# Kernel optimization log

Hardware: AMD Instinct MI355X
Metric: run time of the kernel (lower is better)

## Reference

```python
import jax, jax.numpy as jnp
import numpy as np

EMBED = 768
HEADS = 12
B, S = 32, 1024


def setup_inputs() -> dict:
    key = jax.random.key(0)
    k1, k2, k3 = jax.random.split(key, 3)
    scale_in = 1.0 / np.sqrt(EMBED)
    x = jax.random.normal(k1, (B, S, EMBED), dtype=jnp.float32)
    # weights stored [in, out] (transpose of torch Linear layout)
    w_qkv = jax.random.normal(k2, (EMBED, 3 * EMBED), dtype=jnp.float32) * scale_in
    b_qkv = jnp.zeros((3 * EMBED,), dtype=jnp.float32)
    w_o = jax.random.normal(k3, (EMBED, EMBED), dtype=jnp.float32) * scale_in
    b_o = jnp.zeros((EMBED,), dtype=jnp.float32)
    return {"x": x, "w_qkv": w_qkv, "b_qkv": b_qkv, "w_o": w_o, "b_o": b_o}


def reference(x, w_qkv, b_qkv, w_o, b_o):
    Bt, St, E = x.shape
    H = HEADS
    Dh = E // H
    qkv = x @ w_qkv + b_qkv                      # [B, S, 3E]
    qkv = qkv.reshape(Bt, St, H, 3 * Dh)          # [B, S, H, 3Dh]
    q, k, v = jnp.split(qkv, 3, axis=-1)          # each [B, S, H, Dh]
    # NOTE: faithful to source — attention over the HEADS axis per token,
    # scaled by embed_size**-0.5 (not head_dim**-0.5).
    attn = jnp.einsum('bshd,bsgd->bshg', q, k) * (E ** -0.5)  # [B, S, H, H]
    attn = jax.nn.softmax(attn, axis=-1)
    out = jnp.einsum('bshg,bsgd->bshd', attn, v)  # [B, S, H, Dh]
    out = out.reshape(Bt, St, E)
    return out @ w_o + b_o
```

## Files before the change

kernel.cpp:

```cpp
#include <hip/hip_runtime.h>
#include <hip/hip_bf16.h>

#define EMBED 768
#define HEADS 12
#define TOKENS 32768
#define QKVN  (3*EMBED)
#define KDIM  768
#define NKT   (KDIM/64)
#define QK_SCALE 0.03608439182435161f

typedef __attribute__((ext_vector_type(8))) __bf16 bf16x8;
typedef __attribute__((ext_vector_type(4))) __bf16 bf16x4;
typedef __attribute__((ext_vector_type(4))) float  f32x4;

__device__ __forceinline__ void gload_lds16(const void* gptr, void* lptr) {
    __builtin_amdgcn_global_load_lds(
        (const __attribute__((address_space(1))) void*)gptr,
        (__attribute__((address_space(3))) void*)lptr,
        16, 0, 0);
}

__global__ __launch_bounds__(256) void k_cvt_bf16(const float4* __restrict__ src,
                                                  bf16x4* __restrict__ dst, int n4) {
    int i = blockIdx.x * blockDim.x + threadIdx.x;
    int stride = gridDim.x * blockDim.x;
    for (; i < n4; i += stride) {
        float4 f = src[i];
        bf16x4 o;
        o[0] = (__bf16)f.x; o[1] = (__bf16)f.y; o[2] = (__bf16)f.z; o[3] = (__bf16)f.w;
        dst[i] = o;
    }
}

__global__ __launch_bounds__(256) void k_pack_b(const float* __restrict__ w,
                                                __bf16* __restrict__ BF, int N) {
    int tid = blockIdx.x * 256 + threadIdx.x;
    int lane = tid & 63;
    int rest = tid >> 6;
    int N16 = N >> 4;
    int ks = rest & 1;
    int n16 = (rest >> 1) % N16;
    int kt = (rest >> 1) / N16;
    if (kt >= NKT) return;
    int col = n16 * 16 + (lane & 15);
    int k0 = kt * 64 + ks * 32 + (lane >> 4) * 8;
    bf16x8 o;
#pragma unroll
    for (int e = 0; e < 8; ++e) o[e] = (__bf16)w[(size_t)(k0 + e) * N + col];
    *(bf16x8*)(BF + (size_t)tid * 8) = o;
}

template <typename OutT>
__global__ __launch_bounds__(256, 2) void gemm_bl(const __bf16* __restrict__ A,
                                                  const __bf16* __restrict__ BF,
                                                  const float* __restrict__ bias,
                                                  OutT* __restrict__ C, int N) {
    __shared__ __align__(1024) char lds[49152];
    const int tid = threadIdx.x;
    const int w = tid >> 6, lane = tid & 63;
    const int l15 = lane & 15, l16 = lane >> 4;
    const int K = KDIM;
    const int N16 = N >> 4;
    const long ktstride = (long)N16 * 1024;

    const int nbx = N >> 8;
    const int cpx = gridDim.x >> 3;
    const int bid = blockIdx.x;
    const int swz = (bid & 7) * cpx + (bid >> 3);
    const int brow = swz / nbx, bcol = swz % nbx;
    const long arow0 = (long)brow * 128;
    const int  ncol0 = bcol * 256;

    const __bf16* Asrc = A + (arow0 + w * 8 + (lane >> 3)) * K
                           + (((lane & 7) ^ (lane >> 3)) * 8);
    auto stageA = [&](int slot, int kt) {
#pragma unroll
        for (int j = 0; j < 4; ++j)
            gload_lds16(Asrc + (long)(j * 32) * K + (long)kt * 64,
                        lds + slot * 16384 + j * 4096 + w * 1024 + lane * 16);
    };

    const int cA0 = l15 * 128 + (((0 * 4 + l16) ^ (l15 & 7)) * 16);
    const int cA1 = l15 * 128 + (((1 * 4 + l16) ^ (l15 & 7)) * 16);

    const __bf16* bbase = BF + (size_t)lane * 8 + ((long)(ncol0 >> 4) + w * 4) * 1024;

    f32x4 acc[8][4] = {};
    bf16x8 bfv[8];

#define LOADB(KT, HALF) do { \
    _Pragma("unroll") for (int n = 0; n < 4; ++n) \
        bfv[(HALF) * 4 + n] = *(const bf16x8*)(bbase + (long)(KT) * ktstride + n * 1024 + (HALF) * 512); \
} while (0)

#define VMW12 asm volatile("s_waitcnt vmcnt(12)" ::: "memory")
#define VMW8  asm volatile("s_waitcnt vmcnt(8)"  ::: "memory")

#define KSTEP(SLOT, BKT, AKT, VMW, DOBAR) do { \
    bf16x8 af[16]; \
    _Pragma("unroll") for (int mf = 0; mf < 8; ++mf) \
        af[mf] = *(const bf16x8*)(lds + (SLOT) * 16384 + mf * 2048 + cA0); \
    _Pragma("unroll") for (int mf = 0; mf < 8; ++mf) \
        af[8 + mf] = *(const bf16x8*)(lds + (SLOT) * 16384 + mf * 2048 + cA1); \
    __builtin_amdgcn_s_setprio(1); \
    _Pragma("unroll") for (int mf = 0; mf < 8; ++mf) \
        _Pragma("unroll") for (int n = 0; n < 4; ++n) \
            acc[mf][n] = __builtin_amdgcn_mfma_f32_16x16x32_bf16(af[mf], bfv[n], acc[mf][n], 0, 0, 0); \
    __builtin_amdgcn_s_setprio(0); \
    if ((BKT) >= 0) LOADB(BKT, 0); \
    __builtin_amdgcn_s_setprio(1); \
    _Pragma("unroll") for (int mf = 0; mf < 8; ++mf) \
        _Pragma("unroll") for (int n = 0; n < 4; ++n) \
            acc[mf][n] = __builtin_amdgcn_mfma_f32_16x16x32_bf16(af[8 + mf], bfv[4 + n], acc[mf][n], 0, 0, 0); \
    __builtin_amdgcn_s_setprio(0); \
    if ((BKT) >= 0) LOADB(BKT, 1); \
    if ((AKT) >= 0) stageA((AKT) % 3, (AKT)); \
    VMW; \
    if (DOBAR) { __builtin_amdgcn_s_barrier(); __builtin_amdgcn_sched_barrier(0); } \
} while (0)

    stageA(0, 0);
    LOADB(0, 0); LOADB(0, 1);
    asm volatile("s_waitcnt vmcnt(0)" ::: "memory");
    stageA(1, 1);
    __builtin_amdgcn_s_barrier();
    __builtin_amdgcn_sched_barrier(0);

    for (int t = 0; t < 9; t += 3) {
        KSTEP(0, t + 1, t + 2, VMW12, 1);
        KSTEP(1, t + 2, t + 3, VMW12, 1);
        KSTEP(2, t + 3, t + 4, VMW12, 1);
    }
    KSTEP(0, 10, 11, VMW12, 1);
    KSTEP(1, 11, -1, VMW8, 1);
    KSTEP(2, -1, -1, , 0);
#undef KSTEP
#undef LOADB
#undef VMW12
#undef VMW8

#pragma unroll
    for (int mf = 0; mf < 8; ++mf) {
        const int row = (int)arow0 + mf * 16 + l16 * 4;
#pragma unroll
        for (int n = 0; n < 4; ++n) {
            const int col = ncol0 + w * 64 + n * 16 + l15;
            const float bv = bias[col];
#pragma unroll
            for (int j = 0; j < 4; ++j) {
                C[(long)(row + j) * N + col] = (OutT)(acc[mf][n][j] + bv);
            }
        }
    }
}

#define HPITCH 200
__global__ __launch_bounds__(256) void k_attn(const __bf16* __restrict__ qkv,
                                              __bf16* __restrict__ out) {
    __shared__ __bf16 rows[4][12 * HPITCH];
    __shared__ float wts[4][144];
    const int w = threadIdx.x >> 6, lane = threadIdx.x & 63;
    const long token = (long)blockIdx.x * 4 + w;
    const __bf16* rp = qkv + token * QKVN;
    __bf16* row = rows[w];
    float* wt  = wts[w];

#pragma unroll
    for (int i = 0; i < 4; i++) {
        int c = i * 64 + lane;
        int h = c / 24;
        *(bf16x8*)(row + h * HPITCH + (c * 8 - h * 192)) = *(const bf16x8*)(rp + c * 8);
    }
    if (lane < 32) {
        int c = 256 + lane;
        int h = c / 24;
        *(bf16x8*)(row + h * HPITCH + (c * 8 - h * 192)) = *(const bf16x8*)(rp + c * 8);
    }
    __syncthreads();

    for (int p = lane; p < 144; p += 64) {
        int h = p / 12, g = p - h * 12;
        const __bf16* qp = row + h * HPITCH;
        const __bf16* kp = row + g * HPITCH + 64;
        float s = 0.f;
#pragma unroll
        for (int d = 0; d < 64; d += 8) {
            bf16x8 qv = *(const bf16x8*)(qp + d);
            bf16x8 kv = *(const bf16x8*)(kp + d);
#pragma unroll
            for (int j = 0; j < 8; j++) s += (float)qv[j] * (float)kv[j];
        }
        wt[p] = s * QK_SCALE;
    }
    __syncthreads();

    if (lane < 12) {
        float s[12];
#pragma unroll
        for (int g = 0; g < 12; g++) s[g] = wt[lane * 12 + g];
        float m = s[0];
#pragma unroll
        for (int g = 1; g < 12; g++) m = fmaxf(m, s[g]);
        float sum = 0.f;
#pragma unroll
        for (int g = 0; g < 12; g++) { s[g] = __expf(s[g] - m); sum += s[g]; }
        float inv = 1.0f / sum;
#pragma unroll
        for (int g = 0; g < 12; g++) wt[lane * 12 + g] = s[g] * inv;
    }
    __syncthreads();

    float vr[12];
#pragma unroll
    for (int g = 0; g < 12; g++) vr[g] = (float)row[g * HPITCH + 128 + lane];
#pragma unroll
    for (int h = 0; h < 12; h++) {
        float a = 0.f;
#pragma unroll
        for (int g = 0; g < 12; g++) a += wt[h * 12 + g] * vr[g];
        out[token * EMBED + h * 64 + lane] = (__bf16)a;
    }
}

extern "C" void kernel_launch(void* const* d_in, const int* in_sizes, int n_in,
                              void* d_out, int out_size, void* d_ws, size_t ws_size,
                              hipStream_t stream) {
    const float* x     = (const float*)d_in[0];
    const float* w_qkv = (const float*)d_in[1];
    const float* b_qkv = (const float*)d_in[2];
    const float* w_o   = (const float*)d_in[3];
    const float* b_o   = (const float*)d_in[4];
    float* out = (float*)d_out;

    char* ws = (char*)d_ws;
    size_t off = 0;
    auto take = [&](size_t bytes) {
        char* p = ws + off;
        off += (bytes + 255) & ~(size_t)255;
        return p;
    };
    __bf16* wqkvp = (__bf16*)take((size_t)QKVN * KDIM * 2);
    __bf16* wop   = (__bf16*)take((size_t)EMBED * KDIM * 2);
    __bf16* xb    = (__bf16*)take((size_t)TOKENS * EMBED * 2);
    __bf16* qkvb  = (__bf16*)take((size_t)TOKENS * QKVN * 2);
    __bf16* attno = xb;

    int n4 = TOKENS * EMBED / 4;
    k_cvt_bf16<<<2048, 256, 0, stream>>>((const float4*)x, (bf16x4*)xb, n4);

    k_pack_b<<<(NKT * (QKVN / 16) * 2 * 64) / 256, 256, 0, stream>>>(w_qkv, wqkvp, QKVN);
    k_pack_b<<<(NKT * (EMBED / 16) * 2 * 64) / 256, 256, 0, stream>>>(w_o, wop, EMBED);

    gemm_bl<__bf16><<<(TOKENS / 128) * (QKVN / 256), 256, 0, stream>>>(
        xb, wqkvp, b_qkv, qkvb, QKVN);

    k_attn<<<TOKENS / 4, 256, 0, stream>>>(qkvb, attno);

    gemm_bl<float><<<(TOKENS / 128) * (EMBED / 256), 256, 0, stream>>>(
        attno, wop, b_o, out, EMBED);
}
```

Baseline: 237.4 us.

## Fuse fp32-to-bf16 input conversion into the QKV GEMM A-tile staging

Removes the separate conversion kernel for x. The QKV GEMM now reads fp32 activations straight into registers, converts them to bf16 and writes them to LDS, with a software-pipelined three-slot schedule. This saves one full pass over x (read fp32, write bf16) and one kernel launch. In exchange, the GEMM reads twice as many A bytes per tile and each of the 9 column blocks rereads the same rows, adding register pressure and replacing the async global-to-LDS loads with a synchronous register path.

```diff
diff --git a/kernel.cpp b/kernel.cpp
--- a/kernel.cpp
+++ b/kernel.cpp
@@ -18,18 +18,6 @@
         (const __attribute__((address_space(1))) void*)gptr,
         (__attribute__((address_space(3))) void*)lptr,
         16, 0, 0);
-}
-
-__global__ __launch_bounds__(256) void k_cvt_bf16(const float4* __restrict__ src,
-                                                  bf16x4* __restrict__ dst, int n4) {
-    int i = blockIdx.x * blockDim.x + threadIdx.x;
-    int stride = gridDim.x * blockDim.x;
-    for (; i < n4; i += stride) {
-        float4 f = src[i];
-        bf16x4 o;
-        o[0] = (__bf16)f.x; o[1] = (__bf16)f.y; o[2] = (__bf16)f.z; o[3] = (__bf16)f.w;
-        dst[i] = o;
-    }
 }
 
 __global__ __launch_bounds__(256) void k_pack_b(const float* __restrict__ w,
@@ -50,6 +38,129 @@
     *(bf16x8*)(BF + (size_t)tid * 8) = o;
 }
 
+__global__ __launch_bounds__(256, 2) void gemm_cf(const float* __restrict__ A,
+                                                  const __bf16* __restrict__ BF,
+                                                  const float* __restrict__ bias,
+                                                  __bf16* __restrict__ C, int N) {
+    __shared__ __align__(1024) char lds[49152];
+    const int tid = threadIdx.x;
+    const int w = tid >> 6, lane = tid & 63;
+    const int l15 = lane & 15, l16 = lane >> 4;
+    const int K = KDIM;
+    const int N16 = N >> 4;
+    const long ktstride = (long)N16 * 1024;
+
+    const int nbx = N >> 8;
+    const int cpx = gridDim.x >> 3;
+    const int bid = blockIdx.x;
+    const int swz = (bid & 7) * cpx + (bid >> 3);
+    const int brow = swz / nbx, bcol = swz % nbx;
+    const long arow0 = (long)brow * 128;
+    const int  ncol0 = bcol * 256;
+
+    const float* Afsrc = A + (arow0 + w * 8 + (lane >> 3)) * (long)K
+                           + (((lane & 7) ^ (lane >> 3)) * 8);
+    float4 areg[8];
+
+#define ALOAD(KT) do { \
+    _Pragma("unroll") for (int j = 0; j < 4; ++j) { \
+        areg[j * 2]     = *(const float4*)(Afsrc + (long)(j * 32) * K + (long)(KT) * 64); \
+        areg[j * 2 + 1] = *(const float4*)(Afsrc + (long)(j * 32) * K + (long)(KT) * 64 + 4); \
+    } \
+} while (0)
+
+#define AWRITE(SLOT) do { \
+    _Pragma("unroll") for (int j = 0; j < 4; ++j) { \
+        bf16x8 o; \
+        o[0] = (__bf16)areg[j * 2].x;     o[1] = (__bf16)areg[j * 2].y; \
+        o[2] = (__bf16)areg[j * 2].z;     o[3] = (__bf16)areg[j * 2].w; \
+        o[4] = (__bf16)areg[j * 2 + 1].x; o[5] = (__bf16)areg[j * 2 + 1].y; \
+        o[6] = (__bf16)areg[j * 2 + 1].z; o[7] = (__bf16)areg[j * 2 + 1].w; \
+        *(bf16x8*)(lds + (SLOT) * 16384 + j * 4096 + w * 1024 + lane * 16) = o; \
+    } \
+} while (0)
+
+    const int cA0 = l15 * 128 + (((0 * 4 + l16) ^ (l15 & 7)) * 16);
+    const int cA1 = l15 * 128 + (((1 * 4 + l16) ^ (l15 & 7)) * 16);
+    const __bf16* bbase = BF + (size_t)lane * 8 + ((long)(ncol0 >> 4) + w * 4) * 1024;
+
+    f32x4 acc[8][4] = {};
+    bf16x8 bfv[8];
+
+#define LOADB(KT, HALF) do { \
+    _Pragma("unroll") for (int n = 0; n < 4; ++n) \
+        bfv[(HALF) * 4 + n] = *(const bf16x8*)(bbase + (long)(KT) * ktstride + n * 1024 + (HALF) * 512); \
+} while (0)
+
+#define KSTEP_CF(SLOT, BKT, AWSLOT, ALKT, DOBAR) do { \
+    { \
+        bf16x8 af0[8]; \
+        _Pragma("unroll") for (int mf = 0; mf < 8; ++mf) \
+            af0[mf] = *(const bf16x8*)(lds + (SLOT) * 16384 + mf * 2048 + cA0); \
+        __builtin_amdgcn_s_setprio(1); \
+        _Pragma("unroll") for (int mf = 0; mf < 8; ++mf) \
+            _Pragma("unroll") for (int n = 0; n < 4; ++n) \
+                acc[mf][n] = __builtin_amdgcn_mfma_f32_16x16x32_bf16(af0[mf], bfv[n], acc[mf][n], 0, 0, 0); \
+        __builtin_amdgcn_s_setprio(0); \
+    } \
+    if ((BKT) >= 0) LOADB(BKT, 0); \
+    { \
+        bf16x8 af1[8]; \
+        _Pragma("unroll") for (int mf = 0; mf < 8; ++mf) \
+            af1[mf] = *(const bf16x8*)(lds + (SLOT) * 16384 + mf * 2048 + cA1); \
+        __builtin_amdgcn_s_setprio(1); \
+        _Pragma("unroll") for (int mf = 0; mf < 8; ++mf) \
+            _Pragma("unroll") for (int n = 0; n < 4; ++n) \
+                acc[mf][n] = __builtin_amdgcn_mfma_f32_16x16x32_bf16(af1[mf], bfv[4 + n], acc[mf][n], 0, 0, 0); \
+        __builtin_amdgcn_s_setprio(0); \
+    } \
+    if ((BKT) >= 0) LOADB(BKT, 1); \
+    if ((AWSLOT) >= 0) { \
+        asm volatile("s_waitcnt vmcnt(8)" ::: "memory"); \
+        AWRITE(AWSLOT); \
+    } \
+    if ((ALKT) >= 0) ALOAD(ALKT); \
+    if ((AWSLOT) >= 0) asm volatile("s_waitcnt lgkmcnt(0)" ::: "memory"); \
+    if (DOBAR) { __builtin_amdgcn_s_barrier(); __builtin_amdgcn_sched_barrier(0); } \
+} while (0)
+
+    ALOAD(0);
+    LOADB(0, 0); LOADB(0, 1);
+    asm volatile("s_waitcnt vmcnt(8)" ::: "memory");
+    AWRITE(0);
+    ALOAD(1);
+    asm volatile("s_waitcnt lgkmcnt(0)" ::: "memory");
+    __builtin_amdgcn_s_barrier();
+    __builtin_amdgcn_sched_barrier(0);
+
+    for (int t = 0; t < 9; t += 3) {
+        KSTEP_CF(0, t + 1, (t + 1) % 3, t + 2, 1);
+        KSTEP_CF(1, t + 2, (t + 2) % 3, t + 3, 1);
+        KSTEP_CF(2, t + 3, (t + 3) % 3, t + 4, 1);
+    }
+    KSTEP_CF(0, 10, 1, 11, 1);
+    KSTEP_CF(1, 11, 2, -1, 1);
+    KSTEP_CF(2, -1, -1, -1, 0);
+#undef KSTEP_CF
+#undef ALOAD
+#undef AWRITE
+#undef LOADB
+
+#pragma unroll
+    for (int mf = 0; mf < 8; ++mf) {
+        const int row = (int)arow0 + mf * 16 + l16 * 4;
+#pragma unroll
+        for (int n = 0; n < 4; ++n) {
+            const int col = ncol0 + w * 64 + n * 16 + l15;
+            const float bv = bias[col];
+#pragma unroll
+            for (int j = 0; j < 4; ++j) {
+                C[(long)(row + j) * N + col] = (__bf16)(acc[mf][n][j] + bv);
+            }
+        }
+    }
+}
+
 template <typename OutT>
 __global__ __launch_bounds__(256, 2) void gemm_bl(const __bf16* __restrict__ A,
                                                   const __bf16* __restrict__ BF,
@@ -82,7 +193,6 @@
 
     const int cA0 = l15 * 128 + (((0 * 4 + l16) ^ (l15 & 7)) * 16);
     const int cA1 = l15 * 128 + (((1 * 4 + l16) ^ (l15 & 7)) * 16);
-
     const __bf16* bbase = BF + (size_t)lane * 8 + ((long)(ncol0 >> 4) + w * 4) * 1024;
 
     f32x4 acc[8][4] = {};
@@ -241,18 +351,14 @@
     };
     __bf16* wqkvp = (__bf16*)take((size_t)QKVN * KDIM * 2);
     __bf16* wop   = (__bf16*)take((size_t)EMBED * KDIM * 2);
-    __bf16* xb    = (__bf16*)take((size_t)TOKENS * EMBED * 2);
     __bf16* qkvb  = (__bf16*)take((size_t)TOKENS * QKVN * 2);
-    __bf16* attno = xb;
-
-    int n4 = TOKENS * EMBED / 4;
-    k_cvt_bf16<<<2048, 256, 0, stream>>>((const float4*)x, (bf16x4*)xb, n4);
+    __bf16* attno = (__bf16*)take((size_t)TOKENS * EMBED * 2);
 
     k_pack_b<<<(NKT * (QKVN / 16) * 2 * 64) / 256, 256, 0, stream>>>(w_qkv, wqkvp, QKVN);
     k_pack_b<<<(NKT * (EMBED / 16) * 2 * 64) / 256, 256, 0, stream>>>(w_o, wop, EMBED);
 
-    gemm_bl<__bf16><<<(TOKENS / 128) * (QKVN / 256), 256, 0, stream>>>(
-        xb, wqkvp, b_qkv, qkvb, QKVN);
+    gemm_cf<<<(TOKENS / 128) * (QKVN / 256), 256, 0, stream>>>(
+        x, wqkvp, b_qkv, qkvb, QKVN);
 
     k_attn<<<TOKENS / 4, 256, 0, stream>>>(qkvb, attno);
 
```

Result: slower. 277.1 us (+16.7%).
